# Kernel optimization log

Measured on AMD Instinct MI355X. Metric: run time of the kernel, lower is better.

## Reference

```python
import jax, jax.numpy as jnp
import numpy as np

K = 3          # kernel size
STRIDE = 1
PAD = 1
DIL = 1
BN_EPS = 1e-5


def _conv2d(x, w, b, stride=STRIDE, pad=PAD):
    out = jax.lax.conv_general_dilated(
        x, w, (stride, stride), [(pad, pad), (pad, pad)],
        dimension_numbers=("NCHW", "OIHW", "NCHW"))
    return out + b[None, :, None, None]


def _bilinear_sample(x, py, px):
    """Zero-padded bilinear sampling. x: [B,C,H,W]; py,px: [B,Ho,Wo] float coords."""
    B, C, H, W = x.shape
    y0 = jnp.floor(py)
    x0 = jnp.floor(px)
    wy1 = py - y0
    wx1 = px - x0
    x_flat = x.reshape(B, C, H * W)

    def gather(yi, xi, wgt):
        valid = (yi >= 0) & (yi <= H - 1) & (xi >= 0) & (xi <= W - 1)
        yc = jnp.clip(yi, 0, H - 1).astype(jnp.int32)
        xc = jnp.clip(xi, 0, W - 1).astype(jnp.int32)
        idx = (yc * W + xc).reshape(B, 1, -1)                      # [B,1,Ho*Wo]
        v = jnp.take_along_axis(x_flat, idx, axis=2)               # [B,C,Ho*Wo]
        v = v.reshape(B, C, py.shape[1], py.shape[2])
        return v * (wgt * valid)[:, None]

    return (gather(y0,     x0,     (1 - wy1) * (1 - wx1)) +
            gather(y0,     x0 + 1, (1 - wy1) * wx1) +
            gather(y0 + 1, x0,     wy1 * (1 - wx1)) +
            gather(y0 + 1, x0 + 1, wy1 * wx1))


def _forward(x, off_w, off_b, dc_w, dc_b, bn_gamma, bn_beta, bn_mean, bn_var):
    B, C, H, W = x.shape
    K2 = K * K
    om = _conv2d(x, off_w, off_b)                 # [B, 3*K2, H, W]
    offset = om[:, :2 * K2]                       # interleaved (dy, dx) per tap
    mask = jax.nn.sigmoid(om[:, 2 * K2:])         # [B, K2, H, W]

    # output pixel -> top-left input coordinate of the receptive field
    base_y = (jnp.arange(H) * STRIDE - PAD)[:, None]   # [H,1]
    base_x = (jnp.arange(W) * STRIDE - PAD)[None, :]   # [1,W]

    out = jnp.zeros((B, dc_w.shape[0], H, W), dtype=x.dtype)
    for k in range(K2):
        kh, kw = k // K, k % K
        py = base_y + kh * DIL + offset[:, 2 * k]      # [B,H,W]
        px = base_x + kw * DIL + offset[:, 2 * k + 1]  # [B,H,W]
        samp = _bilinear_sample(x, py, px) * mask[:, k][:, None]
        out = out + jnp.einsum('oc,bchw->bohw', dc_w[:, :, kh, kw], samp)
    out = out + dc_b[None, :, None, None]

    # BatchNorm (inference: running stats) + ReLU
    scale = bn_gamma / jnp.sqrt(bn_var + BN_EPS)
    out = out * scale[None, :, None, None] + (bn_beta - bn_mean * scale)[None, :, None, None]
    return jax.nn.relu(out)


def setup_inputs() -> dict:
    key = jax.random.key(0)
    ks = jax.random.split(key, 8)
    B, Cin, Cout, H, W = 8, 256, 256, 64, 64
    K2 = K * K
    x = jax.random.normal(ks[0], (B, Cin, H, W), dtype=jnp.float32)
    # NOTE: original init zeros the offset conv; we use small random weights so
    # offsets/masks are nontrivial and the bilinear path is exercised.
    off_w = jax.random.normal(ks[1], (3 * K2, Cin, K, K), dtype=jnp.float32) * 0.01
    off_b = jax.random.normal(ks[2], (3 * K2,), dtype=jnp.float32) * 0.01
    dc_w = jax.random.normal(ks[3], (Cout, Cin, K, K), dtype=jnp.float32) / np.sqrt(Cin * K2)
    dc_b = jax.random.normal(ks[4], (Cout,), dtype=jnp.float32) * 0.01
    bn_gamma = jnp.ones((Cout,), dtype=jnp.float32)
    bn_beta = jnp.zeros((Cout,), dtype=jnp.float32)
    bn_mean = jax.random.normal(ks[5], (Cout,), dtype=jnp.float32) * 0.1
    bn_var = jax.random.uniform(ks[6], (Cout,), dtype=jnp.float32) * 0.5 + 0.5
    return {"x": x, "off_w": off_w, "off_b": off_b, "dc_w": dc_w, "dc_b": dc_b,
            "bn_gamma": bn_gamma, "bn_beta": bn_beta,
            "bn_mean": bn_mean, "bn_var": bn_var}


def reference(x, off_w, off_b, dc_w, dc_b, bn_gamma, bn_beta, bn_mean, bn_var):
    return _forward(x, off_w, off_b, dc_w, dc_b, bn_gamma, bn_beta, bn_mean, bn_var)
```

## Files before the change

### kernel.cpp

```cpp
#include <hip/hip_runtime.h>
#include <hip/hip_bf16.h>
#include <cstdint>
#include <cstddef>

#define HH 64
#define WW 64
#define CIN 256
#define COUT 256
#define NB 8
#define HW (HH * WW)
#define BN_EPS 1e-5f

typedef __attribute__((ext_vector_type(8))) short s16x8;
typedef __attribute__((ext_vector_type(8))) unsigned short u16x8;
typedef __attribute__((ext_vector_type(4))) float f32x4;

static __device__ __forceinline__ float bf2f(unsigned short u) {
  unsigned int v = ((unsigned int)u) << 16;
  return __builtin_bit_cast(float, v);
}
static __device__ __forceinline__ unsigned short f2bf(float f) {
  __hip_bfloat16 h = __float2bfloat16(f);
  return __builtin_bit_cast(unsigned short, h);
}
static __device__ __forceinline__ u16x8 shfl32(u16x8 v) {
  int4 a = __builtin_bit_cast(int4, v);
  int4 r;
  r.x = __shfl_xor(a.x, 32, 64);
  r.y = __shfl_xor(a.y, 32, 64);
  r.z = __shfl_xor(a.z, 32, 64);
  r.w = __shfl_xor(a.w, 32, 64);
  return __builtin_bit_cast(u16x8, r);
}

__global__ __launch_bounds__(256) void k_tr(const float* __restrict__ x,
                                            unsigned short* __restrict__ xbf) {
  __shared__ float tile[64][65];
  int bid = blockIdx.x;
  int b = bid & 7;
  int r = bid >> 3;
  int ct = r & 3;
  int st = r >> 2;
  int lane = threadIdx.x & 63;
  int grp = threadIdx.x >> 6;
  int c0 = ct * 64, s0 = st * 64;
  const float* xb = x + (size_t)b * CIN * HW;
#pragma unroll
  for (int i = 0; i < 16; ++i) {
    int row = grp * 16 + i;
    tile[row][lane] = xb[(size_t)(c0 + row) * HW + s0 + lane];
  }
  __syncthreads();
  unsigned short* xo = xbf + (size_t)b * HW * CIN;
#pragma unroll
  for (int i = 0; i < 16; ++i) {
    int row = grp * 16 + i;
    xo[(size_t)(s0 + row) * CIN + c0 + lane] = f2bf(tile[lane][row]);
  }
}

__global__ __launch_bounds__(256) void k_wt(const float* __restrict__ dc_w,
                                            unsigned short* __restrict__ Wf) {
  int idx = blockIdx.x * 256 + threadIdx.x;
  if (idx >= 9 * 8 * 16 * 64 * 8) return;
  int j = idx & 7;
  int lane = (idx >> 3) & 63;
  int tile = (idx >> 9) & 15;
  int ks = (idx >> 13) & 7;
  int k = idx >> 16;
  int o = tile * 16 + (lane & 15);
  int c = ks * 32 + (lane >> 4) * 8 + j;
  Wf[idx] = f2bf(dc_w[((size_t)o * CIN + c) * 9 + k]);
}

__global__ __launch_bounds__(256) void k_owt(const float* __restrict__ off_w,
                                             unsigned short* __restrict__ OWf) {
  int idx = blockIdx.x * 256 + threadIdx.x;
  if (idx >= 9 * 8 * 2 * 64 * 8) return;
  int j = idx & 7;
  int lane = (idx >> 3) & 63;
  int kot = (idx >> 9) & 1;
  int ks = (idx >> 10) & 7;
  int t = idx >> 13;
  int ko = kot * 16 + (lane & 15);
  int c = ks * 32 + (lane >> 4) * 8 + j;
  unsigned short v = 0;
  if (ko < 27) v = f2bf(off_w[((size_t)ko * CIN + c) * 9 + t]);
  OWf[idx] = v;
}

__global__ void k_bn(const float* __restrict__ g, const float* __restrict__ be,
                     const float* __restrict__ m, const float* __restrict__ va,
                     const float* __restrict__ db, float* __restrict__ sc,
                     float* __restrict__ bi) {
  int o = threadIdx.x;
  float s = g[o] * rsqrtf(va[o] + BN_EPS);
  sc[o] = s;
  bi[o] = be[o] + (db[o] - m[o]) * s;
}

__global__ __launch_bounds__(256, 2) void k_main(
    const unsigned short* __restrict__ xbf, const unsigned short* __restrict__ OWf,
    const float* __restrict__ off_b, const unsigned short* __restrict__ Wf,
    const float* __restrict__ bnsc, const float* __restrict__ bnbi,
    float* __restrict__ out) {
  int bid = blockIdx.x;
  int b = bid & 7;
  int h = bid >> 3;
  int tid = threadIdx.x;
  int lane = tid & 63;
  int wave = tid >> 6;
  int l15 = lane & 15, l4 = lane >> 4;

  __shared__ __align__(16) unsigned short ubuf[66 * 256];
  __shared__ float om_lds[27][64];
  __shared__ int pre_off[9][64][4];
  __shared__ float pre_w[9][64][4];

  const unsigned short* xb = xbf + (size_t)b * HW * CIN;

  if (tid < 64) {
    int r = (tid < 32) ? 0 : 65;
    int ch = tid & 31;
    u16x8 z = {0, 0, 0, 0, 0, 0, 0, 0};
    *(u16x8*)&ubuf[r * 256 + ch * 8] = z;
  }

  f32x4 acc_oc[2];
  acc_oc[0] = (f32x4){0.f, 0.f, 0.f, 0.f};
  acc_oc[1] = (f32x4){0.f, 0.f, 0.f, 0.f};
  int wavepx = wave * 16;

  for (int kh = 0; kh < 3; ++kh) {
    int y = h + kh - 1;
    if (y < 0 || y >= HH) continue;
    __syncthreads();
    const unsigned short* src = xb + (size_t)y * WW * CIN;
#pragma unroll
    for (int i = 0; i < 8; ++i) {
      int e8 = i * 256 + tid;
      int px = e8 >> 5;
      int ch = e8 & 31;
      u16x8 v = *(const u16x8*)(src + e8 * 8);
      *(u16x8*)&ubuf[(px + 1) * 256 + ((ch ^ ((px + 1) & 7)) * 8)] = v;
    }
    __syncthreads();
#pragma unroll
    for (int kw = 0; kw < 3; ++kw) {
      int prow = wavepx + l15 + kw;
      int rs = prow & 7;
      const unsigned short* Atap = OWf + ((size_t)(kh * 3 + kw) * 8) * 1024 + lane * 8;
#pragma unroll
      for (int ks = 0; ks < 8; ++ks) {
        s16x8 bfrag = *(const s16x8*)&ubuf[prow * 256 + (((ks * 4 + l4) ^ rs) * 8)];
#pragma unroll
        for (int kot = 0; kot < 2; ++kot) {
          s16x8 afrag = *(const s16x8*)(Atap + ks * 1024 + kot * 512);
          acc_oc[kot] = __builtin_amdgcn_mfma_f32_16x16x32_bf16(afrag, bfrag,
                                                                acc_oc[kot], 0, 0, 0);
        }
      }
    }
  }
#pragma unroll
  for (int kot = 0; kot < 2; ++kot) {
#pragma unroll
    for (int j = 0; j < 4; ++j) {
      int ko = kot * 16 + l4 * 4 + j;
      if (ko < 27) om_lds[ko][wavepx + l15] = acc_oc[kot][j];
    }
  }
  __syncthreads();

  for (int item = tid; item < 9 * 64; item += 256) {
    int k = item >> 6;
    int w = item & 63;
    int kh = k / 3, kw = k % 3;
    float offy = om_lds[2 * k][w] + off_b[2 * k];
    float offx = om_lds[2 * k + 1][w] + off_b[2 * k + 1];
    float mk = om_lds[18 + k][w] + off_b[18 + k];
    mk = 1.0f / (1.0f + expf(-mk));
    float py = (float)(h - 1 + kh) + offy;
    float px = (float)(w - 1 + kw) + offx;
    float fy0 = floorf(py), fx0 = floorf(px);
    float wy1 = py - fy0, wx1 = px - fx0;
    int y0 = (int)fy0, x0 = (int)fx0;
    int y1 = y0 + 1, x1 = x0 + 1;
    bool vy0 = (y0 >= 0) && (y0 <= HH - 1);
    bool vy1 = (y1 >= 0) && (y1 <= HH - 1);
    bool vx0 = (x0 >= 0) && (x0 <= WW - 1);
    bool vx1 = (x1 >= 0) && (x1 <= WW - 1);
    int y0c = min(max(y0, 0), HH - 1), y1c = min(max(y1, 0), HH - 1);
    int x0c = min(max(x0, 0), WW - 1), x1c = min(max(x1, 0), WW - 1);
    pre_w[k][w][0] = (1.f - wy1) * (1.f - wx1) * mk * ((vy0 && vx0) ? 1.f : 0.f);
    pre_w[k][w][1] = (1.f - wy1) * wx1 * mk * ((vy0 && vx1) ? 1.f : 0.f);
    pre_w[k][w][2] = wy1 * (1.f - wx1) * mk * ((vy1 && vx0) ? 1.f : 0.f);
    pre_w[k][w][3] = wy1 * wx1 * mk * ((vy1 && vx1) ? 1.f : 0.f);
    pre_off[k][w][0] = (y0c * WW + x0c) * CIN;
    pre_off[k][w][1] = (y0c * WW + x1c) * CIN;
    pre_off[k][w][2] = (y1c * WW + x0c) * CIN;
    pre_off[k][w][3] = (y1c * WW + x1c) * CIN;
  }

  unsigned short(*S)[256] = (unsigned short(*)[256])ubuf;
  f32x4 acc[4][4];
#pragma unroll
  for (int i = 0; i < 4; ++i)
#pragma unroll
    for (int j = 0; j < 4; ++j) acc[i][j] = (f32x4){0.f, 0.f, 0.f, 0.f};

  int pswz = lane & 7;
  int o_base = wave * 64;
  int half = lane >> 5;
  int chunk = lane & 31;

  for (int k = 0; k < 9; ++k) {
    __syncthreads();
    {
#pragma unroll 4
      for (int pp = 0; pp < 16; ++pp) {
        int px = wavepx + pp;
        int oA = pre_off[k][px][half];
        float wA = pre_w[k][px][half];
        int oB = pre_off[k][px][2 + half];
        float wB = pre_w[k][px][2 + half];
        u16x8 vA = *(const u16x8*)(xb + oA + chunk * 8);
        u16x8 vB = *(const u16x8*)(xb + oB + chunk * 8);
        u16x8 sA = shfl32(vA);
        u16x8 sB = shfl32(vB);
        float wsA = __shfl_xor(wA, 32, 64);
        float wsB = __shfl_xor(wB, 32, 64);
        u16x8 r;
#pragma unroll
        for (int j = 0; j < 8; ++j) {
          float s = wA * bf2f(vA[j]) + wsA * bf2f(sA[j]) + wB * bf2f(vB[j]) +
                    wsB * bf2f(sB[j]);
          r[j] = f2bf(s);
        }
        if (lane < 32) {
          int phys = (chunk & 24) | ((chunk ^ px) & 7);
          *(u16x8*)&S[px][phys * 8] = r;
        }
      }
    }
    __syncthreads();
    const unsigned short* Wa = Wf + (size_t)k * 65536 + (wave * 4) * 512 + lane * 8;
#pragma unroll
    for (int ks = 0; ks < 8; ++ks) {
      s16x8 a[4], bf[4];
#pragma unroll
      for (int ot = 0; ot < 4; ++ot)
        a[ot] = *(const s16x8*)(Wa + ks * 8192 + ot * 512);
#pragma unroll
      for (int pt = 0; pt < 4; ++pt) {
        int slot = (ks * 4 + l4) ^ pswz;
        bf[pt] = *(const s16x8*)&S[pt * 16 + l15][slot * 8];
      }
#pragma unroll
      for (int ot = 0; ot < 4; ++ot)
#pragma unroll
        for (int pt = 0; pt < 4; ++pt)
          acc[ot][pt] = __builtin_amdgcn_mfma_f32_16x16x32_bf16(a[ot], bf[pt],
                                                                acc[ot][pt], 0, 0, 0);
    }
  }

#pragma unroll
  for (int ot = 0; ot < 4; ++ot) {
#pragma unroll
    for (int j = 0; j < 4; ++j) {
      int o = o_base + ot * 16 + l4 * 4 + j;
      float sc = bnsc[o], bi = bnbi[o];
      float* ob = out + (((size_t)b * COUT + o) * HH + h) * WW;
#pragma unroll
      for (int pt = 0; pt < 4; ++pt) {
        ob[pt * 16 + l15] = fmaxf(fmaf(acc[ot][pt][j], sc, bi), 0.f);
      }
    }
  }
}

extern "C" void kernel_launch(void* const* d_in, const int* in_sizes, int n_in,
                              void* d_out, int out_size, void* d_ws, size_t ws_size,
                              hipStream_t stream) {
  const float* x = (const float*)d_in[0];
  const float* off_w = (const float*)d_in[1];
  const float* off_b = (const float*)d_in[2];
  const float* dc_w = (const float*)d_in[3];
  const float* dc_b = (const float*)d_in[4];
  const float* bn_gamma = (const float*)d_in[5];
  const float* bn_beta = (const float*)d_in[6];
  const float* bn_mean = (const float*)d_in[7];
  const float* bn_var = (const float*)d_in[8];
  float* out = (float*)d_out;

  char* ws = (char*)d_ws;
  unsigned short* xbf = (unsigned short*)ws;
  ws += (size_t)NB * HW * CIN * sizeof(unsigned short);
  unsigned short* Wf = (unsigned short*)ws;
  ws += (size_t)9 * 8 * 16 * 64 * 8 * sizeof(unsigned short);
  unsigned short* OWf = (unsigned short*)ws;
  ws += (size_t)9 * 8 * 2 * 64 * 8 * sizeof(unsigned short);
  float* bnsc = (float*)ws;
  ws += 256 * sizeof(float);
  float* bnbi = (float*)ws;

  k_tr<<<NB * 64 * 4, 256, 0, stream>>>(x, xbf);
  k_wt<<<(9 * 8 * 16 * 64 * 8 + 255) / 256, 256, 0, stream>>>(dc_w, Wf);
  k_owt<<<(9 * 8 * 2 * 64 * 8 + 255) / 256, 256, 0, stream>>>(off_w, OWf);
  k_bn<<<1, 256, 0, stream>>>(bn_gamma, bn_beta, bn_mean, bn_var, dc_b, bnsc, bnbi);
  k_main<<<NB * HH, 256, 0, stream>>>(xbf, OWf, off_b, Wf, bnsc, bnbi, out);
}
```

Before: 128.7 us.

## Gather four bilinear corners per lane, halving pixels per wave and dropping shuffles

The bilinear gather loop now has each half-wave handle its own pixel, with each lane loading all four corner vectors directly. This replaces the earlier scheme where half the lanes loaded two corners and exchanged them through cross-lane shuffles, and where only half the lanes wrote to LDS. The precomputed offsets and weights are shrunk to 16-bit indices and fp16 weights to cut LDS use, and launch bounds are raised to allow three blocks per CU. The risks are fp16 rounding of the bilinear weights, a higher register-pressure cap, and more global loads in flight per lane.

```diff
diff --git a/kernel.cpp b/kernel.cpp
--- a/kernel.cpp
+++ b/kernel.cpp
@@ -1,5 +1,6 @@
 #include <hip/hip_runtime.h>
 #include <hip/hip_bf16.h>
+#include <hip/hip_fp16.h>
 #include <cstdint>
 #include <cstddef>
 
@@ -22,15 +23,6 @@
 static __device__ __forceinline__ unsigned short f2bf(float f) {
   __hip_bfloat16 h = __float2bfloat16(f);
   return __builtin_bit_cast(unsigned short, h);
-}
-static __device__ __forceinline__ u16x8 shfl32(u16x8 v) {
-  int4 a = __builtin_bit_cast(int4, v);
-  int4 r;
-  r.x = __shfl_xor(a.x, 32, 64);
-  r.y = __shfl_xor(a.y, 32, 64);
-  r.z = __shfl_xor(a.z, 32, 64);
-  r.w = __shfl_xor(a.w, 32, 64);
-  return __builtin_bit_cast(u16x8, r);
 }
 
 __global__ __launch_bounds__(256) void k_tr(const float* __restrict__ x,
@@ -99,7 +91,7 @@
   bi[o] = be[o] + (db[o] - m[o]) * s;
 }
 
-__global__ __launch_bounds__(256, 2) void k_main(
+__global__ __launch_bounds__(256, 3) void k_main(
     const unsigned short* __restrict__ xbf, const unsigned short* __restrict__ OWf,
     const float* __restrict__ off_b, const unsigned short* __restrict__ Wf,
     const float* __restrict__ bnsc, const float* __restrict__ bnbi,
@@ -114,8 +106,8 @@
 
   __shared__ __align__(16) unsigned short ubuf[66 * 256];
   __shared__ float om_lds[27][64];
-  __shared__ int pre_off[9][64][4];
-  __shared__ float pre_w[9][64][4];
+  __shared__ unsigned short pre_offS[9][64][4];
+  __shared__ __half pre_wH[9][64][4];
 
   const unsigned short* xb = xbf + (size_t)b * HW * CIN;
 
@@ -192,14 +184,15 @@
     bool vx1 = (x1 >= 0) && (x1 <= WW - 1);
     int y0c = min(max(y0, 0), HH - 1), y1c = min(max(y1, 0), HH - 1);
     int x0c = min(max(x0, 0), WW - 1), x1c = min(max(x1, 0), WW - 1);
-    pre_w[k][w][0] = (1.f - wy1) * (1.f - wx1) * mk * ((vy0 && vx0) ? 1.f : 0.f);
-    pre_w[k][w][1] = (1.f - wy1) * wx1 * mk * ((vy0 && vx1) ? 1.f : 0.f);
-    pre_w[k][w][2] = wy1 * (1.f - wx1) * mk * ((vy1 && vx0) ? 1.f : 0.f);
-    pre_w[k][w][3] = wy1 * wx1 * mk * ((vy1 && vx1) ? 1.f : 0.f);
-    pre_off[k][w][0] = (y0c * WW + x0c) * CIN;
-    pre_off[k][w][1] = (y0c * WW + x1c) * CIN;
-    pre_off[k][w][2] = (y1c * WW + x0c) * CIN;
-    pre_off[k][w][3] = (y1c * WW + x1c) * CIN;
+    pre_wH[k][w][0] =
+        __float2half((1.f - wy1) * (1.f - wx1) * mk * ((vy0 && vx0) ? 1.f : 0.f));
+    pre_wH[k][w][1] = __float2half((1.f - wy1) * wx1 * mk * ((vy0 && vx1) ? 1.f : 0.f));
+    pre_wH[k][w][2] = __float2half(wy1 * (1.f - wx1) * mk * ((vy1 && vx0) ? 1.f : 0.f));
+    pre_wH[k][w][3] = __float2half(wy1 * wx1 * mk * ((vy1 && vx1) ? 1.f : 0.f));
+    pre_offS[k][w][0] = (unsigned short)(y0c * WW + x0c);
+    pre_offS[k][w][1] = (unsigned short)(y0c * WW + x1c);
+    pre_offS[k][w][2] = (unsigned short)(y1c * WW + x0c);
+    pre_offS[k][w][3] = (unsigned short)(y1c * WW + x1c);
   }
 
   unsigned short(*S)[256] = (unsigned short(*)[256])ubuf;
@@ -211,36 +204,36 @@
 
   int pswz = lane & 7;
   int o_base = wave * 64;
-  int half = lane >> 5;
+  int hv = lane >> 5;
   int chunk = lane & 31;
 
   for (int k = 0; k < 9; ++k) {
     __syncthreads();
     {
-#pragma unroll 4
-      for (int pp = 0; pp < 16; ++pp) {
-        int px = wavepx + pp;
-        int oA = pre_off[k][px][half];
-        float wA = pre_w[k][px][half];
-        int oB = pre_off[k][px][2 + half];
-        float wB = pre_w[k][px][2 + half];
-        u16x8 vA = *(const u16x8*)(xb + oA + chunk * 8);
-        u16x8 vB = *(const u16x8*)(xb + oB + chunk * 8);
-        u16x8 sA = shfl32(vA);
-        u16x8 sB = shfl32(vB);
-        float wsA = __shfl_xor(wA, 32, 64);
-        float wsB = __shfl_xor(wB, 32, 64);
+#pragma unroll
+      for (int pp = 0; pp < 8; ++pp) {
+        int px = wavepx + pp * 2 + hv;
+        int i0 = ((int)pre_offS[k][px][0]) << 8;
+        int i1 = ((int)pre_offS[k][px][1]) << 8;
+        int i2 = ((int)pre_offS[k][px][2]) << 8;
+        int i3 = ((int)pre_offS[k][px][3]) << 8;
+        float w0 = __half2float(pre_wH[k][px][0]);
+        float w1 = __half2float(pre_wH[k][px][1]);
+        float w2 = __half2float(pre_wH[k][px][2]);
+        float w3 = __half2float(pre_wH[k][px][3]);
+        u16x8 v0 = *(const u16x8*)(xb + i0 + chunk * 8);
+        u16x8 v1 = *(const u16x8*)(xb + i1 + chunk * 8);
+        u16x8 v2 = *(const u16x8*)(xb + i2 + chunk * 8);
+        u16x8 v3 = *(const u16x8*)(xb + i3 + chunk * 8);
         u16x8 r;
 #pragma unroll
         for (int j = 0; j < 8; ++j) {
-          float s = wA * bf2f(vA[j]) + wsA * bf2f(sA[j]) + wB * bf2f(vB[j]) +
-                    wsB * bf2f(sB[j]);
+          float s = w0 * bf2f(v0[j]) + w1 * bf2f(v1[j]) + w2 * bf2f(v2[j]) +
+                    w3 * bf2f(v3[j]);
           r[j] = f2bf(s);
         }
-        if (lane < 32) {
-          int phys = (chunk & 24) | ((chunk ^ px) & 7);
-          *(u16x8*)&S[px][phys * 8] = r;
-        }
+        int phys = chunk ^ (px & 7);
+        *(u16x8*)&S[px][phys * 8] = r;
       }
     }
     __syncthreads();
```

New measurement: 107.4 us. 1.2x faster.
